# Kernel optimization log

Measured on AMD Instinct MI355X. Metric: run time of the kernel, lower is better.

The kernel has to match this reference:

```python
import jax, jax.numpy as jnp
import numpy as np

B, L, C, S, W, R = 2, 16, 64, 64, 128, 32
MOD_HIDDEN = 32


def _conv3d(x, k, b, pad_hw):
    # x: (B,C,L,S,W), k: (O,I,1,kh,kw)
    y = jax.lax.conv_general_dilated(
        x, k, window_strides=(1, 1, 1),
        padding=((0, 0), (pad_hw, pad_hw), (pad_hw, pad_hw)),
        dimension_numbers=('NCDHW', 'OIDHW', 'NCDHW'))
    return y + b[None, :, None, None, None]


def setup_inputs() -> dict:
    key = jax.random.key(0)
    ks = jax.random.split(key, 16)
    d = {}
    d['x'] = jax.random.normal(ks[0], (B, L, C, S, W), jnp.float32)
    u1 = jax.random.uniform(ks[1], (C, R), jnp.float32)
    u2 = jax.random.uniform(ks[2], (C, R), jnp.float32)
    r_min, r_max = 0.8, 0.99
    d['nu_log'] = jnp.log(-0.5 * jnp.log(u1 * (r_max ** 2 - r_min ** 2) + r_min ** 2))
    d['theta_log'] = jnp.log(u2 * jnp.float32(2 * np.pi))
    d['disp_nu'] = jnp.zeros((C, R), jnp.float32)
    d['disp_theta'] = jnp.zeros((C, R), jnp.float32)
    d['mlp_w1'] = jax.random.normal(ks[3], (C, MOD_HIDDEN), jnp.float32) / np.sqrt(C).astype(np.float32)
    d['mlp_b1'] = jnp.zeros((MOD_HIDDEN,), jnp.float32)
    d['mlp_w2'] = jax.random.normal(ks[4], (MOD_HIDDEN, C * R * 2), jnp.float32) / np.sqrt(MOD_HIDDEN).astype(np.float32)
    d['mlp_b2'] = jnp.zeros((C * R * 2,), jnp.float32)
    d['forcing_scale'] = jnp.float32(0.1)
    d['U_row_r'] = jax.random.normal(ks[5], (C, S, R), jnp.float32) / np.sqrt(S).astype(np.float32)
    d['U_row_i'] = jax.random.normal(ks[6], (C, S, R), jnp.float32) / np.sqrt(S).astype(np.float32)
    d['V_col_r'] = jax.random.normal(ks[7], (C, W, R), jnp.float32) / np.sqrt(W).astype(np.float32)
    d['V_col_i'] = jax.random.normal(ks[8], (C, W, R), jnp.float32) / np.sqrt(W).astype(np.float32)
    d['proj_W_r'] = jax.random.normal(ks[9], (C, C), jnp.float32) / np.sqrt(C).astype(np.float32)
    d['proj_W_i'] = jax.random.normal(ks[10], (C, C), jnp.float32) / np.sqrt(C).astype(np.float32)
    d['proj_b_r'] = jnp.zeros((C,), jnp.float32)
    d['proj_b_i'] = jnp.zeros((C,), jnp.float32)
    fan = np.sqrt(C * 9).astype(np.float32)
    d['convr_k'] = jax.random.normal(ks[11], (C, C, 1, 3, 3), jnp.float32) / fan
    d['convr_b'] = jnp.zeros((C,), jnp.float32)
    d['convi_k'] = jax.random.normal(ks[12], (C, C, 1, 3, 3), jnp.float32) / fan
    d['convi_b'] = jnp.zeros((C,), jnp.float32)
    d['fuse_k'] = jax.random.normal(ks[13], (C, 2 * C, 1, 1, 1), jnp.float32) / np.sqrt(2 * C).astype(np.float32)
    d['fuse_b'] = jnp.zeros((C,), jnp.float32)
    d['ln_g'] = jnp.ones((S, W), jnp.float32)
    d['ln_b'] = jnp.zeros((S, W), jnp.float32)
    return d


def reference(x, nu_log, theta_log, disp_nu, disp_theta, mlp_w1, mlp_b1,
              mlp_w2, mlp_b2, forcing_scale, U_row_r, U_row_i, V_col_r,
              V_col_i, proj_W_r, proj_W_i, proj_b_r, proj_b_i, convr_k,
              convr_b, convi_k, convi_b, fuse_k, fuse_b, ln_g, ln_b):
    # Diagonal LRU poles lam = exp(-exp(nu) + i*exp(theta)), per (C,R)
    nu = jnp.exp(nu_log + disp_nu)
    theta = jnp.exp(theta_log + disp_theta)
    lam = jnp.exp(jax.lax.complex(-nu, theta))
    gamma = jnp.sqrt(jnp.clip(1.0 - jnp.abs(lam) ** 2, 1e-6, None))

    # Selective input-dependent forcing from spatially-pooled context
    ctx = x.mean(axis=(-2, -1))  # (B,L,C)
    f = jnp.tanh(ctx @ mlp_w1 + mlp_b1) @ mlp_w2 + mlp_b2
    f = f.reshape(ctx.shape[0], ctx.shape[1], C, R, 2)
    forcing = forcing_scale * jax.lax.complex(f[..., 0], f[..., 1])  # (B,L,C,R)

    # Low-rank complex spatial projection to rank-R state per channel
    U = jax.lax.complex(U_row_r, U_row_i)  # (C,S,R)
    V = jax.lax.complex(V_col_r, V_col_i)  # (C,W,R)
    xc = x.astype(jnp.complex64)
    u = jnp.einsum('blcsw,csr->blcwr', xc, jnp.conj(U))
    u = jnp.einsum('blcwr,cwr->blcr', u, jnp.conj(V))  # (B,L,C,R)
    u = gamma * u * (1.0 + forcing)

    # Diagonal linear recurrence h_t = lam*h_{t-1} + u_t via associative scan over L
    A = jnp.broadcast_to(lam[None, None], u.shape)

    def comb(e1, e2):
        a1, b1 = e1
        a2, b2 = e2
        return a1 * a2, a2 * b1 + b2

    _, h = jax.lax.associative_scan(comb, (A, u), axis=1)

    # Reconstruct spatial field from low-rank states
    t = jnp.einsum('blcr,csr->blcsr', h, U)
    y = jnp.einsum('blcsr,cwr->blcsw', t, V)  # (B,L,C,S,W) complex

    projW = jax.lax.complex(proj_W_r, proj_W_i)
    projb = jax.lax.complex(proj_b_r, proj_b_i)
    y = jnp.einsum('blcsw,oc->blosw', y, projW) + projb[None, None, :, None, None]

    # Post-recurrence spatial convs on real/imag parts, fuse, layernorm, residual
    yr = jnp.transpose(jnp.real(y), (0, 2, 1, 3, 4))  # (B,C,L,S,W)
    yi = jnp.transpose(jnp.imag(y), (0, 2, 1, 3, 4))
    yr = _conv3d(yr, convr_k, convr_b, 1)
    yi = _conv3d(yi, convi_k, convi_b, 1)
    fused = _conv3d(jnp.concatenate([yr, yi], axis=1), fuse_k, fuse_b, 0)
    fused = jnp.transpose(fused, (0, 2, 1, 3, 4))  # (B,L,C,S,W)

    mu = fused.mean(axis=(-2, -1), keepdims=True)
    var = fused.var(axis=(-2, -1), keepdims=True)
    normed = (fused - mu) / jnp.sqrt(var + 1e-5) * ln_g + ln_b
    return normed + x
```

## Files before the change

### kernel.cpp

```cpp
#include <hip/hip_runtime.h>

typedef unsigned short u16;
typedef unsigned int u32;
typedef __attribute__((ext_vector_type(8))) short short8;
typedef __attribute__((ext_vector_type(4))) float f32x4;
typedef __attribute__((ext_vector_type(16))) float f32x16;

constexpr int B = 2, L = 16, C = 64, S = 64, W = 128, R = 32, MH = 32;
constexpr int BL = B * L;
constexpr int SW = S * W;
constexpr int CR = C * R;
constexpr int F2 = C * R * 2;
constexpr int NVE = 64 * 4 * 4 * 64 * 8;
constexpr int NVD = 64 * 8 * 2 * 64 * 8;

__device__ __forceinline__ float us2f(u16 h) { return __uint_as_float(((u32)h) << 16); }
__device__ __forceinline__ float bf_lo(u32 u) { return __uint_as_float(u << 16); }
__device__ __forceinline__ float bf_hi(u32 u) { return __uint_as_float(u & 0xffff0000u); }
__device__ __forceinline__ u16 f2bu(float f) {
  u32 u = __float_as_uint(f);
  u32 r = (u + 0x7fffu + ((u >> 16) & 1u)) >> 16;
  return (u16)r;
}
__device__ __forceinline__ u32 pack2(float lo, float hi) {
  return (u32)f2bu(lo) | ((u32)f2bu(hi) << 16);
}

__global__ void k_prep(const float* __restrict__ nu_log, const float* __restrict__ th_log,
                       const float* __restrict__ dnu, const float* __restrict__ dth,
                       float* __restrict__ lamr, float* __restrict__ lami,
                       float* __restrict__ gam) {
  int i = blockIdx.x * 256 + threadIdx.x;
  if (i >= CR) return;
  float nu = expf(nu_log[i] + dnu[i]);
  float th = expf(th_log[i] + dth[i]);
  float mag = expf(-nu);
  lamr[i] = mag * cosf(th);
  lami[i] = mag * sinf(th);
  gam[i] = sqrtf(fmaxf(1.0f - mag * mag, 1e-6f));
}

__global__ void k_keff(const float* __restrict__ fuse_k, const float* __restrict__ fuse_b,
                       const float* __restrict__ convr_k, const float* __restrict__ convr_b,
                       const float* __restrict__ convi_k, const float* __restrict__ convi_b,
                       u16* __restrict__ keff_bf, float* __restrict__ biaseff) {
  int i = blockIdx.x * 256 + threadIdx.x;
  if (i < C * 2 * C * 9) {
    int o = i / (2 * C * 9);
    int rem = i - o * (2 * C * 9);
    int cin2 = rem / 9;
    int seg = rem - cin2 * 9;
    const float* ck = (cin2 < C) ? convr_k : convi_k;
    int cin = cin2 & (C - 1);
    int fbase = o * 2 * C + ((cin2 < C) ? 0 : C);
    float acc = 0.f;
    for (int m = 0; m < C; ++m)
      acc += fuse_k[fbase + m] * ck[(m * C + cin) * 9 + seg];
    int kslice = cin2 >> 4;
    int kk = cin2 & 15;
    int lane = (o & 31) | ((kk >> 3) << 5);
    int j = kk & 7;
    int m_tile = o >> 5;
    keff_bf[((((seg * 8 + kslice) * 2 + m_tile) * 64 + lane) << 3) + j] = f2bu(acc);
  } else if (i < C * 2 * C * 9 + C) {
    int o = i - C * 2 * C * 9;
    float acc = fuse_b[o];
    for (int m = 0; m < C; ++m) {
      acc += fuse_k[o * 2 * C + m] * convr_b[m];
      acc += fuse_k[o * 2 * C + C + m] * convi_b[m];
    }
    biaseff[o] = acc;
  }
}

__global__ void k_vpack(const float* __restrict__ Vr, const float* __restrict__ Vi,
                        u16* __restrict__ venc, u16* __restrict__ vdecr,
                        u16* __restrict__ vdeci) {
  int i = blockIdx.x * 256 + threadIdx.x;
  if (i < NVE) {
    int j = i & 7, lane = (i >> 3) & 63, ks = (i >> 9) & 3;
    int wv = (i >> 11) & 3, c = i >> 13;
    int n = wv * 16 + (lane & 15);
    int w = ks * 32 + ((lane >> 4) & 3) * 8 + j;
    float v = (n < 32) ? Vr[(size_t)c * 4096 + w * 32 + n]
                       : -Vi[(size_t)c * 4096 + w * 32 + (n - 32)];
    venc[i] = f2bu(v);
  } else if (i < NVE + 2 * NVD) {
    int ii = i - NVE;
    int isI = 0;
    if (ii >= NVD) { ii -= NVD; isI = 1; }
    int j = ii & 7, lane = (ii >> 3) & 63, ks = (ii >> 9) & 1;
    int g = (ii >> 10) & 7, c = ii >> 13;
    int w = g * 16 + (lane & 15);
    int k = ks * 32 + ((lane >> 4) & 3) * 8 + j;
    float v;
    if (!isI) v = (k < 32) ? Vr[(size_t)c * 4096 + w * 32 + k]
                           : -Vi[(size_t)c * 4096 + w * 32 + (k - 32)];
    else      v = (k < 32) ? Vi[(size_t)c * 4096 + w * 32 + k]
                           :  Vr[(size_t)c * 4096 + w * 32 + (k - 32)];
    (isI ? vdeci : vdecr)[ii] = f2bu(v);
  }
}

__global__ void k_apack(const float* __restrict__ pWr, const float* __restrict__ pWi,
                        u16* __restrict__ aproj) {
  int i = blockIdx.x * 256 + threadIdx.x;
  if (i >= 128 * 128) return;
  int m = i >> 7, k = i & 127;
  int c = k >> 1, im = k & 1;
  int o = m & 63;
  float v;
  if (m < 64) v = im ? -pWi[o * 64 + c] : pWr[o * 64 + c];
  else        v = im ?  pWr[o * 64 + c] : pWi[o * 64 + c];
  aproj[i] = f2bu(v);
}

__global__ __launch_bounds__(256) void k_mlp(
    const float* __restrict__ ctx, const float* __restrict__ w1, const float* __restrict__ b1,
    const float* __restrict__ w2, const float* __restrict__ b2, const float* __restrict__ fscale,
    float* __restrict__ forcing) {
  int bl = blockIdx.x >> 4;
  int kt = blockIdx.x & 15;
  int k0 = kt * 256;
  __shared__ float cv[C];
  __shared__ float hid[MH];
  __shared__ float lw2[MH * 256];
  int t = threadIdx.x;
  if (t < C) cv[t] = ctx[bl * C + t];
  for (int i = t; i < MH * 64; i += 256) {
    int j = i >> 6, q = i & 63;
    ((float4*)lw2)[i] = ((const float4*)(w2 + (size_t)j * F2 + k0))[q];
  }
  __syncthreads();
  if (t < MH) {
    float a = b1[t];
    for (int c2 = 0; c2 < C; ++c2) a += cv[c2] * w1[c2 * MH + t];
    hid[t] = tanhf(a);
  }
  __syncthreads();
  float scale = fscale[0];
  float a = b2[k0 + t];
#pragma unroll
  for (int j = 0; j < MH; ++j) a += hid[j] * lw2[j * 256 + t];
  forcing[(size_t)bl * F2 + k0 + t] = scale * a;
}

__global__ __launch_bounds__(256) void k_enc(
    const float* __restrict__ x, const u16* __restrict__ venc,
    const float* __restrict__ Ur, const float* __restrict__ Ui,
    float* __restrict__ ctx, float* __restrict__ u) {
  int blc = blockIdx.x;
  int c = blc & (C - 1);
  __shared__ __align__(16) char smem[35968];
  u16* xt = (u16*)smem;
  float* uldr = (float*)(smem + 17408);
  float* uldi = uldr + 2048;
  float* y1  = (float*)smem;
  float* part = (float*)(smem + 33792);
  float* red = (float*)(smem + 35840);
  int t = threadIdx.x;
  int lane = t & 63, wv = t >> 6;
  short8 bf[4];
  {
    const short8* vep = (const short8*)venc + ((size_t)(c * 4 + wv) * 4) * 64 + lane;
#pragma unroll
    for (int ks = 0; ks < 4; ++ks) bf[ks] = vep[ks * 64];
  }
  float sm = 0.f;
  {
    const float4* xp = (const float4*)(x + (size_t)blc * SW);
    for (int i = t; i < SW / 4; i += 256) {
      float4 v = xp[i];
      sm += v.x + v.y + v.z + v.w;
      int idx = i * 4, s = idx >> 7, w = idx & 127;
      u32* d = (u32*)&xt[s * 136 + w];
      d[0] = pack2(v.x, v.y);
      d[1] = pack2(v.z, v.w);
    }
  }
#pragma unroll
  for (int o = 32; o > 0; o >>= 1) sm += __shfl_down(sm, o, 64);
  if (lane == 0) red[wv] = sm;
  {
    const float* urp = Ur + (size_t)c * 2048;
    const float* uip = Ui + (size_t)c * 2048;
    for (int i = t; i < 2048; i += 256) { uldr[i] = urp[i]; uldi[i] = uip[i]; }
  }
  __syncthreads();
  if (t == 0) ctx[blc] = (red[0] + red[1] + red[2] + red[3]) * (1.f / SW);
  int quad = lane >> 4, l15 = lane & 15;
  f32x4 zf = {0.f, 0.f, 0.f, 0.f};
  f32x4 acc[4] = {zf, zf, zf, zf};
#pragma unroll
  for (int ks = 0; ks < 4; ++ks) {
    int kofs = ks * 32 + quad * 8;
#pragma unroll
    for (int mt = 0; mt < 4; ++mt) {
      short8 af = *(const short8*)&xt[(mt * 16 + l15) * 136 + kofs];
      acc[mt] = __builtin_amdgcn_mfma_f32_16x16x32_bf16(af, bf[ks], acc[mt], 0, 0, 0);
    }
  }
  __syncthreads();
#pragma unroll
  for (int mt = 0; mt < 4; ++mt)
#pragma unroll
    for (int reg = 0; reg < 4; ++reg)
      y1[(mt * 16 + quad * 4 + reg) * 65 + wv * 16 + l15] = acc[mt][reg];
  __syncthreads();
  {
    int r = t & 31, sg = t >> 5;
    float pr = 0.f, pi = 0.f;
#pragma unroll
    for (int k = 0; k < 8; ++k) {
      int s = sg * 8 + k;
      float yr = y1[s * 65 + r], yi = y1[s * 65 + 32 + r];
      float ur = uldr[s * 32 + r], ui = uldi[s * 32 + r];
      pr += ur * yr + ui * yi;
      pi += ur * yi - ui * yr;
    }
    part[sg * 64 + r * 2]     = pr;
    part[sg * 64 + r * 2 + 1] = pi;
  }
  __syncthreads();
  if (t < 32) {
    float pr = 0.f, pi = 0.f;
#pragma unroll
    for (int sg = 0; sg < 8; ++sg) {
      pr += part[sg * 64 + t * 2];
      pi += part[sg * 64 + t * 2 + 1];
    }
    u[((size_t)blc * R + t) * 2]     = pr;
    u[((size_t)blc * R + t) * 2 + 1] = pi;
  }
}

__global__ void k_scan(const float* __restrict__ lamr, const float* __restrict__ lami,
                       const float* __restrict__ gam, const float* __restrict__ forcing,
                       const float* __restrict__ u, float* __restrict__ h) {
  int i = blockIdx.x * 256 + threadIdx.x;
  if (i >= B * CR) return;
  int b = i / CR;
  int cr = i - b * CR;
  float lr = lamr[cr], li = lami[cr], g = gam[cr];
  float hr = 0.f, hi = 0.f;
  for (int l = 0; l < L; ++l) {
    size_t off = ((size_t)(b * L + l) * CR + cr) * 2;
    float ur0 = u[off], ui0 = u[off + 1];
    float fr = forcing[off], fi = forcing[off + 1];
    float ofr = 1.f + fr;
    float ur = g * (ur0 * ofr - ui0 * fi);
    float ui = g * (ur0 * fi + ui0 * ofr);
    float nr = lr * hr - li * hi + ur;
    float ni = lr * hi + li * hr + ui;
    hr = nr; hi = ni;
    h[off] = hr; h[off + 1] = hi;
  }
}

__global__ __launch_bounds__(256) void k_decode(
    const float* __restrict__ h,
    const float* __restrict__ Ur, const float* __restrict__ Ui,
    const u16* __restrict__ vdecr, const u16* __restrict__ vdeci,
    u32* __restrict__ y_cm32, int bl_base) {
  int bid = blockIdx.x;
  int c = bid & 63;
  int blh = bid >> 6;
  int bl = bl_base + blh;
  __shared__ __align__(16) u16 ldA[64 * 72];
  int t = threadIdx.x;
  {
    const float* hp = h + ((size_t)(bl * C + c) * R) * 2;
    const float* urp = Ur + (size_t)c * (S * R);
    const float* uip = Ui + (size_t)c * (S * R);
    for (int p = t; p < S * R; p += 256) {
      int s = p >> 5, r = p & 31;
      float hr = hp[r * 2], hi = hp[r * 2 + 1];
      float ur = urp[p], ui = uip[p];
      ldA[s * 72 + r]      = f2bu(hr * ur - hi * ui);
      ldA[s * 72 + 32 + r] = f2bu(hr * ui + hi * ur);
    }
  }
  __syncthreads();
  int lane = t & 63, q = t >> 6;
  int quad = lane >> 4, l15 = lane & 15;
  const short8* vdr = (const short8*)vdecr + (size_t)c * 16 * 64;
  const short8* vdi = (const short8*)vdeci + (size_t)c * 16 * 64;
  f32x4 zf = {0.f, 0.f, 0.f, 0.f};
  f32x4 accr[4][2], acci[4][2];
#pragma unroll
  for (int mt = 0; mt < 4; ++mt)
#pragma unroll
    for (int nt = 0; nt < 2; ++nt) { accr[mt][nt] = zf; acci[mt][nt] = zf; }
#pragma unroll
  for (int ks = 0; ks < 2; ++ks) {
    int kofs = ks * 32 + quad * 8;
    short8 af[4];
#pragma unroll
    for (int mt = 0; mt < 4; ++mt)
      af[mt] = *(const short8*)&ldA[(mt * 16 + l15) * 72 + kofs];
#pragma unroll
    for (int nt = 0; nt < 2; ++nt) {
      int g = q * 2 + nt;
      short8 br = vdr[(g * 2 + ks) * 64 + lane];
      short8 bi = vdi[(g * 2 + ks) * 64 + lane];
#pragma unroll
      for (int mt = 0; mt < 4; ++mt) {
        accr[mt][nt] = __builtin_amdgcn_mfma_f32_16x16x32_bf16(af[mt], br, accr[mt][nt], 0, 0, 0);
        acci[mt][nt] = __builtin_amdgcn_mfma_f32_16x16x32_bf16(af[mt], bi, acci[mt][nt], 0, 0, 0);
      }
    }
  }
  u32* dst = y_cm32 + ((size_t)(blh * 64 + c) << 13);
#pragma unroll
  for (int mt = 0; mt < 4; ++mt) {
#pragma unroll
    for (int nt = 0; nt < 2; ++nt) {
      int w = q * 32 + nt * 16 + l15;
#pragma unroll
      for (int reg = 0; reg < 4; ++reg) {
        int s = mt * 16 + quad * 4 + reg;
        dst[s * 128 + w] = pack2(accr[mt][nt][reg], acci[mt][nt][reg]);
      }
    }
  }
}

__global__ __launch_bounds__(256) void k_proj(
    const u32* __restrict__ y_cm32, const u16* __restrict__ aproj,
    const float* __restrict__ pbr, const float* __restrict__ pbi,
    u16* __restrict__ ynhwc, int bl_base) {
  int bid = blockIdx.x;
  int ntile = bid & 15;
  int blh = bid >> 4;
  int bl = bl_base + blh;
  __shared__ __align__(16) u16 lda[128 * 136];
  __shared__ __align__(16) u32 ldb[128 * 68];
  __shared__ float ldbias[128];
  int t = threadIdx.x;
  for (int i = t; i < 128 * 16; i += 256) {
    int m = i >> 4, qq = i & 15;
    ((uint4*)&lda[m * 136])[qq] = ((const uint4*)&aproj[m * 128])[qq];
  }
  if (t < 128) ldbias[t] = t < 64 ? pbr[t] : pbi[t - 64];

  int lane = t & 63, wv = t >> 6;
  int quad = lane >> 4, l15 = lane & 15;
  int cidx = t & 63, seg = t >> 6;
  f32x4 zf = {0.f, 0.f, 0.f, 0.f};

  for (int chunk = 0; chunk < 4; ++chunk) {
    int n0 = ntile * 512 + chunk * 128;
    __syncthreads();
    {
      const uint4* src = (const uint4*)(y_cm32 + (((size_t)(blh * 64 + cidx)) << 13) + n0 + seg * 32);
      u32 tmp[32];
#pragma unroll
      for (int qq = 0; qq < 8; ++qq) {
        uint4 v = src[qq];
        tmp[qq * 4] = v.x; tmp[qq * 4 + 1] = v.y; tmp[qq * 4 + 2] = v.z; tmp[qq * 4 + 3] = v.w;
      }
#pragma unroll
      for (int j = 0; j < 32; ++j)
        ldb[(seg * 32 + j) * 68 + cidx] = tmp[j];
    }
    __syncthreads();
    f32x4 acc[8][2];
#pragma unroll
    for (int mt = 0; mt < 8; ++mt) { acc[mt][0] = zf; acc[mt][1] = zf; }
    const u16* ldb16 = (const u16*)ldb;
#pragma unroll
    for (int ks = 0; ks < 4; ++ks) {
      int kofs = ks * 32 + quad * 8;
      short8 af[8];
#pragma unroll
      for (int mt = 0; mt < 8; ++mt)
        af[mt] = *(const short8*)&lda[(mt * 16 + l15) * 136 + kofs];
#pragma unroll
      for (int nt = 0; nt < 2; ++nt) {
        int nrow = wv * 32 + nt * 16 + l15;
        short8 bf = *(const short8*)&ldb16[nrow * 136 + kofs];
#pragma unroll
        for (int mt = 0; mt < 8; ++mt)
          acc[mt][nt] = __builtin_amdgcn_mfma_f32_16x16x32_bf16(af[mt], bf, acc[mt][nt], 0, 0, 0);
      }
    }
#pragma unroll
    for (int nt = 0; nt < 2; ++nt) {
      int n = n0 + wv * 32 + nt * 16 + l15;
      u16* drow = ynhwc + (((size_t)bl * SW + n) << 7);
#pragma unroll
      for (int mt = 0; mt < 8; ++mt) {
        int ch = mt * 16 + quad * 4;
        u32 lo = pack2(acc[mt][nt][0] + ldbias[ch],     acc[mt][nt][1] + ldbias[ch + 1]);
        u32 hi = pack2(acc[mt][nt][2] + ldbias[ch + 2], acc[mt][nt][3] + ldbias[ch + 3]);
        u32* dp = (u32*)(drow + ch);
        dp[0] = lo; dp[1] = hi;
      }
    }
  }
}

__global__ __launch_bounds__(256, 4) void k_conv(
    const u16* __restrict__ ynhwc, const u16* __restrict__ keff_bf,
    const float* __restrict__ biaseff, u16* __restrict__ fused) {
  int bid = blockIdx.x;
  int wt = bid & 1;
  int st = (bid >> 1) & 31;
  int bl = bid >> 6;
  int s0 = st * 2;
  int w0 = wt * 64;
  __shared__ __align__(16) u16 win[4][66][72];
  int t = threadIdx.x;
  int c_lo = (wt == 0) ? 1 : 0;
  int c_hi = (wt == 0) ? 66 : 65;
  uint4 z4 = make_uint4(0u, 0u, 0u, 0u);

  int lane = t & 63;
  int wv = t >> 6;
  int sr = wv & 1;
  int mt = wv >> 1;
  int l31 = lane & 31, khalf = lane >> 5;

  f32x16 acc0, acc1;
#pragma unroll
  for (int i = 0; i < 16; ++i) { acc0[i] = 0.f; acc1[i] = 0.f; }
  const short8* ap = (const short8*)keff_bf;
  short8 abuf[2];

#pragma unroll
  for (int p = 0; p < 2; ++p) {
    if (p) __syncthreads();
    for (int rr = 0; rr < 4; ++rr) {
      int rs = s0 - 1 + rr;
      if (rs < 0 || rs >= S) {
        for (int i = t; i < 66 * 8; i += 256) {
          int col = i >> 3, q = i & 7;
          ((uint4*)&win[rr][col][0])[q] = z4;
        }
      } else {
        if (wt == 0 && t < 8) ((uint4*)&win[rr][0][0])[t] = z4;
        if (wt == 1 && t < 8) ((uint4*)&win[rr][65][0])[t] = z4;
        const uint4* src = (const uint4*)(ynhwc +
            (((size_t)bl * S + rs) * W + (w0 - 1 + c_lo)) * 128 + p * 64);
        int n4 = (c_hi - c_lo) * 8;
        for (int i = t; i < n4; i += 256) {
          int col = i >> 3, q = i & 7;
          ((uint4*)&win[rr][c_lo + col][0])[q] = src[col * 16 + q];
        }
      }
    }
    __syncthreads();

    abuf[0] = ap[((p * 4) * 2 + mt) * 64 + lane];

#pragma unroll
    for (int m = 0; m < 36; ++m) {
      const int cur = m & 1;
      const int nxt = cur ^ 1;
      if (m < 35) {
        const int m1 = m + 1;
        abuf[nxt] = ap[((((m1 >> 2) * 8 + p * 4 + (m1 & 3)) * 2 + mt)) * 64 + lane];
      }
      const int seg = m >> 2;
      const int k4 = m & 3;
      const int dr = seg / 3;
      const int dc = seg - dr * 3;
      const u16* bb = &win[sr + dr][l31 + dc][k4 * 16 + khalf * 8];
      short8 b0 = *(const short8*)bb;
      short8 b1 = *(const short8*)(bb + 32 * 72);
      acc0 = __builtin_amdgcn_mfma_f32_32x32x16_bf16(abuf[cur], b0, acc0, 0, 0, 0);
      acc1 = __builtin_amdgcn_mfma_f32_32x32x16_bf16(abuf[cur], b1, acc1, 0, 0, 0);
    }
  }

  int s_out = s0 + sr;
#pragma unroll
  for (int reg = 0; reg < 16; ++reg) {
    int o = mt * 32 + (reg & 3) + 8 * (reg >> 2) + 4 * khalf;
    float bias = biaseff[o];
    size_t rowoff = ((size_t)(bl * C + o) * S + s_out) * W;
    fused[rowoff + w0 + l31]      = f2bu(acc0[reg] + bias);
    fused[rowoff + w0 + 32 + l31] = f2bu(acc1[reg] + bias);
  }
}

__global__ __launch_bounds__(256) void k_ln(
    const u16* __restrict__ fused,
    const float* __restrict__ ln_g, const float* __restrict__ ln_b,
    const float* __restrict__ x, float* __restrict__ out) {
  int blc = blockIdx.x;
  __shared__ u16 fs[SW];
  __shared__ float red[12];
  int t = threadIdx.x;
  const uint4* fp = (const uint4*)(fused + (size_t)blc * SW);
  float sm = 0.f, sq = 0.f;
  for (int i = t; i < SW / 8; i += 256) {
    uint4 v = fp[i];
    ((uint4*)fs)[i] = v;
    float f0 = bf_lo(v.x), f1 = bf_hi(v.x), f2 = bf_lo(v.y), f3 = bf_hi(v.y);
    float f4 = bf_lo(v.z), f5 = bf_hi(v.z), f6 = bf_lo(v.w), f7 = bf_hi(v.w);
    sm += f0 + f1 + f2 + f3 + f4 + f5 + f6 + f7;
    sq += f0 * f0 + f1 * f1 + f2 * f2 + f3 * f3 + f4 * f4 + f5 * f5 + f6 * f6 + f7 * f7;
  }
#pragma unroll
  for (int off = 32; off > 0; off >>= 1) {
    sm += __shfl_down(sm, off, 64);
    sq += __shfl_down(sq, off, 64);
  }
  int lane = t & 63, wid = t >> 6;
  if (lane == 0) { red[wid * 2] = sm; red[wid * 2 + 1] = sq; }
  __syncthreads();
  if (t == 0) {
    float S1 = red[0] + red[2] + red[4] + red[6];
    float S2 = red[1] + red[3] + red[5] + red[7];
    float mu = S1 * (1.f / SW);
    float var = S2 * (1.f / SW) - mu * mu;
    red[8] = mu;
    red[9] = rsqrtf(var + 1e-5f);
  }
  __syncthreads();
  float mu = red[8], rstd = red[9];
  const float4* xp4 = (const float4*)(x + (size_t)blc * SW);
  float4* op4 = (float4*)(out + (size_t)blc * SW);
  const float4* g4 = (const float4*)ln_g;
  const float4* b4 = (const float4*)ln_b;
  const uint2* fs2 = (const uint2*)fs;
  for (int i = t; i < SW / 4; i += 256) {
    uint2 fv = fs2[i];
    float4 xv = xp4[i];
    float4 gv = g4[i];
    float4 bv = b4[i];
    float4 o;
    o.x = (bf_lo(fv.x) - mu) * rstd * gv.x + bv.x + xv.x;
    o.y = (bf_hi(fv.x) - mu) * rstd * gv.y + bv.y + xv.y;
    o.z = (bf_lo(fv.y) - mu) * rstd * gv.z + bv.z + xv.z;
    o.w = (bf_hi(fv.y) - mu) * rstd * gv.w + bv.w + xv.w;
    op4[i] = o;
  }
}

extern "C" void kernel_launch(void* const* d_in, const int* in_sizes, int n_in,
                              void* d_out, int out_size, void* d_ws, size_t ws_size,
                              hipStream_t stream) {
  (void)in_sizes; (void)n_in; (void)out_size; (void)ws_size;
  const float* x       = (const float*)d_in[0];
  const float* nu_log  = (const float*)d_in[1];
  const float* th_log  = (const float*)d_in[2];
  const float* dnu     = (const float*)d_in[3];
  const float* dth     = (const float*)d_in[4];
  const float* w1      = (const float*)d_in[5];
  const float* b1      = (const float*)d_in[6];
  const float* w2      = (const float*)d_in[7];
  const float* b2      = (const float*)d_in[8];
  const float* fscale  = (const float*)d_in[9];
  const float* Ur      = (const float*)d_in[10];
  const float* Ui      = (const float*)d_in[11];
  const float* Vr      = (const float*)d_in[12];
  const float* Vi      = (const float*)d_in[13];
  const float* pWr     = (const float*)d_in[14];
  const float* pWi     = (const float*)d_in[15];
  const float* pbr     = (const float*)d_in[16];
  const float* pbi     = (const float*)d_in[17];
  const float* convr_k = (const float*)d_in[18];
  const float* convr_b = (const float*)d_in[19];
  const float* convi_k = (const float*)d_in[20];
  const float* convi_b = (const float*)d_in[21];
  const float* fuse_k  = (const float*)d_in[22];
  const float* fuse_b  = (const float*)d_in[23];
  const float* ln_g    = (const float*)d_in[24];
  const float* ln_b    = (const float*)d_in[25];
  float* out = (float*)d_out;

  char* ws = (char*)d_ws;
  float* lamr    = (float*)ws;
  float* lami    = lamr + 2048;
  float* gam     = lami + 2048;
  float* biaseff = gam + 2048;
  float* ctx     = biaseff + 64;
  float* forcing = ctx + 2048;
  float* ubuf    = forcing + 131072;
  float* hbuf    = ubuf + 131072;
  u16* keff_bf   = (u16*)(hbuf + 131072);
  u16* aproj     = keff_bf + 73728;
  u16* venc      = aproj + 16384;
  u16* vdecr     = venc + NVE;
  u16* vdeci     = vdecr + NVD;
  size_t off = ((size_t)((char*)(vdeci + NVD) - ws) + 255) & ~(size_t)255;
  u32* y_cm32    = (u32*)(ws + off);
  u16* fused     = (u16*)y_cm32;
  u16* ynhwc     = (u16*)(ws + off + (size_t)32 * 1024 * 1024);

  k_prep<<<8, 256, 0, stream>>>(nu_log, th_log, dnu, dth, lamr, lami, gam);
  k_keff<<<289, 256, 0, stream>>>(fuse_k, fuse_b, convr_k, convr_b, convi_k, convi_b,
                                  keff_bf, biaseff);
  k_vpack<<<6144, 256, 0, stream>>>(Vr, Vi, venc, vdecr, vdeci);
  k_apack<<<64, 256, 0, stream>>>(pWr, pWi, aproj);
  k_enc<<<BL * C, 256, 0, stream>>>(x, venc, Ur, Ui, ctx, ubuf);
  k_mlp<<<BL * 16, 256, 0, stream>>>(ctx, w1, b1, w2, b2, fscale, forcing);
  k_scan<<<16, 256, 0, stream>>>(lamr, lami, gam, forcing, ubuf, hbuf);
  k_decode<<<1024, 256, 0, stream>>>(hbuf, Ur, Ui, vdecr, vdeci, y_cm32, 0);
  k_proj<<<256, 256, 0, stream>>>(y_cm32, aproj, pbr, pbi, ynhwc, 0);
  k_decode<<<1024, 256, 0, stream>>>(hbuf, Ur, Ui, vdecr, vdeci, y_cm32, 16);
  k_proj<<<256, 256, 0, stream>>>(y_cm32, aproj, pbr, pbi, ynhwc, 16);
  k_conv<<<2048, 256, 0, stream>>>(ynhwc, keff_bf, biaseff, fused);
  k_ln<<<BL * C, 256, 0, stream>>>(fused, ln_g, ln_b, x, out);
}
```

Before: 338.8 us.

## Merge prep kernels into one launch, stage scan through LDS, vectorize U loads

The four weight-preparation kernels are merged into a single launch that dispatches on block index, cutting three kernel launches. The scan kernel now stages u and forcing for a block of 128 channels into shared memory with coalesced loads, runs the recurrence from LDS, and writes h back coalesced, using 32 blocks instead of 16. The encoder's U loads switch to float4. Together these target launch overhead and uncoalesced strided access in the scan, at the cost of half the scan threads sitting idle during the recurrence.

```diff
diff --git a/kernel.cpp b/kernel.cpp
--- a/kernel.cpp
+++ b/kernel.cpp
@@ -14,6 +14,12 @@
 constexpr int NVE = 64 * 4 * 4 * 64 * 8;
 constexpr int NVD = 64 * 8 * 2 * 64 * 8;
 
+constexpr int NB_PREP  = 8;
+constexpr int NB_KEFF  = 289;
+constexpr int NB_APACK = 64;
+constexpr int NB_VPACK = (NVE + 2 * NVD + 255) / 256;
+constexpr int NB_ALL   = NB_PREP + NB_KEFF + NB_APACK + NB_VPACK;
+
 __device__ __forceinline__ float us2f(u16 h) { return __uint_as_float(((u32)h) << 16); }
 __device__ __forceinline__ float bf_lo(u32 u) { return __uint_as_float(u << 16); }
 __device__ __forceinline__ float bf_hi(u32 u) { return __uint_as_float(u & 0xffff0000u); }
@@ -26,93 +32,93 @@
   return (u32)f2bu(lo) | ((u32)f2bu(hi) << 16);
 }
 
-__global__ void k_prep(const float* __restrict__ nu_log, const float* __restrict__ th_log,
-                       const float* __restrict__ dnu, const float* __restrict__ dth,
-                       float* __restrict__ lamr, float* __restrict__ lami,
-                       float* __restrict__ gam) {
-  int i = blockIdx.x * 256 + threadIdx.x;
-  if (i >= CR) return;
-  float nu = expf(nu_log[i] + dnu[i]);
-  float th = expf(th_log[i] + dth[i]);
-  float mag = expf(-nu);
-  lamr[i] = mag * cosf(th);
-  lami[i] = mag * sinf(th);
-  gam[i] = sqrtf(fmaxf(1.0f - mag * mag, 1e-6f));
-}
-
-__global__ void k_keff(const float* __restrict__ fuse_k, const float* __restrict__ fuse_b,
-                       const float* __restrict__ convr_k, const float* __restrict__ convr_b,
-                       const float* __restrict__ convi_k, const float* __restrict__ convi_b,
-                       u16* __restrict__ keff_bf, float* __restrict__ biaseff) {
-  int i = blockIdx.x * 256 + threadIdx.x;
-  if (i < C * 2 * C * 9) {
-    int o = i / (2 * C * 9);
-    int rem = i - o * (2 * C * 9);
-    int cin2 = rem / 9;
-    int seg = rem - cin2 * 9;
-    const float* ck = (cin2 < C) ? convr_k : convi_k;
-    int cin = cin2 & (C - 1);
-    int fbase = o * 2 * C + ((cin2 < C) ? 0 : C);
-    float acc = 0.f;
-    for (int m = 0; m < C; ++m)
-      acc += fuse_k[fbase + m] * ck[(m * C + cin) * 9 + seg];
-    int kslice = cin2 >> 4;
-    int kk = cin2 & 15;
-    int lane = (o & 31) | ((kk >> 3) << 5);
-    int j = kk & 7;
-    int m_tile = o >> 5;
-    keff_bf[((((seg * 8 + kslice) * 2 + m_tile) * 64 + lane) << 3) + j] = f2bu(acc);
-  } else if (i < C * 2 * C * 9 + C) {
-    int o = i - C * 2 * C * 9;
-    float acc = fuse_b[o];
-    for (int m = 0; m < C; ++m) {
-      acc += fuse_k[o * 2 * C + m] * convr_b[m];
-      acc += fuse_k[o * 2 * C + C + m] * convi_b[m];
-    }
-    biaseff[o] = acc;
-  }
-}
-
-__global__ void k_vpack(const float* __restrict__ Vr, const float* __restrict__ Vi,
-                        u16* __restrict__ venc, u16* __restrict__ vdecr,
-                        u16* __restrict__ vdeci) {
-  int i = blockIdx.x * 256 + threadIdx.x;
-  if (i < NVE) {
-    int j = i & 7, lane = (i >> 3) & 63, ks = (i >> 9) & 3;
-    int wv = (i >> 11) & 3, c = i >> 13;
-    int n = wv * 16 + (lane & 15);
-    int w = ks * 32 + ((lane >> 4) & 3) * 8 + j;
-    float v = (n < 32) ? Vr[(size_t)c * 4096 + w * 32 + n]
-                       : -Vi[(size_t)c * 4096 + w * 32 + (n - 32)];
-    venc[i] = f2bu(v);
-  } else if (i < NVE + 2 * NVD) {
-    int ii = i - NVE;
-    int isI = 0;
-    if (ii >= NVD) { ii -= NVD; isI = 1; }
-    int j = ii & 7, lane = (ii >> 3) & 63, ks = (ii >> 9) & 1;
-    int g = (ii >> 10) & 7, c = ii >> 13;
-    int w = g * 16 + (lane & 15);
-    int k = ks * 32 + ((lane >> 4) & 3) * 8 + j;
+__global__ void k_prep_all(
+    const float* __restrict__ nu_log, const float* __restrict__ th_log,
+    const float* __restrict__ dnu, const float* __restrict__ dth,
+    float* __restrict__ lamr, float* __restrict__ lami, float* __restrict__ gam,
+    const float* __restrict__ fuse_k, const float* __restrict__ fuse_b,
+    const float* __restrict__ convr_k, const float* __restrict__ convr_b,
+    const float* __restrict__ convi_k, const float* __restrict__ convi_b,
+    u16* __restrict__ keff_bf, float* __restrict__ biaseff,
+    const float* __restrict__ pWr, const float* __restrict__ pWi,
+    u16* __restrict__ aproj,
+    const float* __restrict__ Vr, const float* __restrict__ Vi,
+    u16* __restrict__ venc, u16* __restrict__ vdecr, u16* __restrict__ vdeci) {
+  int bid = blockIdx.x;
+  int t = threadIdx.x;
+  if (bid < NB_PREP) {
+    int i = bid * 256 + t;
+    if (i >= CR) return;
+    float nu = expf(nu_log[i] + dnu[i]);
+    float th = expf(th_log[i] + dth[i]);
+    float mag = expf(-nu);
+    lamr[i] = mag * cosf(th);
+    lami[i] = mag * sinf(th);
+    gam[i] = sqrtf(fmaxf(1.0f - mag * mag, 1e-6f));
+  } else if (bid < NB_PREP + NB_KEFF) {
+    int i = (bid - NB_PREP) * 256 + t;
+    if (i < C * 2 * C * 9) {
+      int o = i / (2 * C * 9);
+      int rem = i - o * (2 * C * 9);
+      int cin2 = rem / 9;
+      int seg = rem - cin2 * 9;
+      const float* ck = (cin2 < C) ? convr_k : convi_k;
+      int cin = cin2 & (C - 1);
+      int fbase = o * 2 * C + ((cin2 < C) ? 0 : C);
+      float acc = 0.f;
+      for (int m = 0; m < C; ++m)
+        acc += fuse_k[fbase + m] * ck[(m * C + cin) * 9 + seg];
+      int kslice = cin2 >> 4;
+      int kk = cin2 & 15;
+      int lane = (o & 31) | ((kk >> 3) << 5);
+      int j = kk & 7;
+      int m_tile = o >> 5;
+      keff_bf[((((seg * 8 + kslice) * 2 + m_tile) * 64 + lane) << 3) + j] = f2bu(acc);
+    } else if (i < C * 2 * C * 9 + C) {
+      int o = i - C * 2 * C * 9;
+      float acc = fuse_b[o];
+      for (int m = 0; m < C; ++m) {
+        acc += fuse_k[o * 2 * C + m] * convr_b[m];
+        acc += fuse_k[o * 2 * C + C + m] * convi_b[m];
+      }
+      biaseff[o] = acc;
+    }
+  } else if (bid < NB_PREP + NB_KEFF + NB_APACK) {
+    int i = (bid - NB_PREP - NB_KEFF) * 256 + t;
+    if (i >= 128 * 128) return;
+    int m = i >> 7, k = i & 127;
+    int c = k >> 1, im = k & 1;
+    int o = m & 63;
     float v;
-    if (!isI) v = (k < 32) ? Vr[(size_t)c * 4096 + w * 32 + k]
-                           : -Vi[(size_t)c * 4096 + w * 32 + (k - 32)];
-    else      v = (k < 32) ? Vi[(size_t)c * 4096 + w * 32 + k]
-                           :  Vr[(size_t)c * 4096 + w * 32 + (k - 32)];
-    (isI ? vdeci : vdecr)[ii] = f2bu(v);
-  }
-}
-
-__global__ void k_apack(const float* __restrict__ pWr, const float* __restrict__ pWi,
-                        u16* __restrict__ aproj) {
-  int i = blockIdx.x * 256 + threadIdx.x;
-  if (i >= 128 * 128) return;
-  int m = i >> 7, k = i & 127;
-  int c = k >> 1, im = k & 1;
-  int o = m & 63;
-  float v;
-  if (m < 64) v = im ? -pWi[o * 64 + c] : pWr[o * 64 + c];
-  else        v = im ?  pWr[o * 64 + c] : pWi[o * 64 + c];
-  aproj[i] = f2bu(v);
+    if (m < 64) v = im ? -pWi[o * 64 + c] : pWr[o * 64 + c];
+    else        v = im ?  pWr[o * 64 + c] : pWi[o * 64 + c];
+    aproj[i] = f2bu(v);
+  } else {
+    int i = (bid - NB_PREP - NB_KEFF - NB_APACK) * 256 + t;
+    if (i < NVE) {
+      int j = i & 7, lane = (i >> 3) & 63, ks = (i >> 9) & 3;
+      int wv = (i >> 11) & 3, c = i >> 13;
+      int n = wv * 16 + (lane & 15);
+      int w = ks * 32 + ((lane >> 4) & 3) * 8 + j;
+      float v = (n < 32) ? Vr[(size_t)c * 4096 + w * 32 + n]
+                         : -Vi[(size_t)c * 4096 + w * 32 + (n - 32)];
+      venc[i] = f2bu(v);
+    } else if (i < NVE + 2 * NVD) {
+      int ii = i - NVE;
+      int isI = 0;
+      if (ii >= NVD) { ii -= NVD; isI = 1; }
+      int j = ii & 7, lane = (ii >> 3) & 63, ks = (ii >> 9) & 1;
+      int g = (ii >> 10) & 7, c = ii >> 13;
+      int w = g * 16 + (lane & 15);
+      int k = ks * 32 + ((lane >> 4) & 3) * 8 + j;
+      float v;
+      if (!isI) v = (k < 32) ? Vr[(size_t)c * 4096 + w * 32 + k]
+                             : -Vi[(size_t)c * 4096 + w * 32 + (k - 32)];
+      else      v = (k < 32) ? Vi[(size_t)c * 4096 + w * 32 + k]
+                             :  Vr[(size_t)c * 4096 + w * 32 + (k - 32)];
+      (isI ? vdeci : vdecr)[ii] = f2bu(v);
+    }
+  }
 }
 
 __global__ __launch_bounds__(256) void k_mlp(
@@ -182,9 +188,11 @@
   for (int o = 32; o > 0; o >>= 1) sm += __shfl_down(sm, o, 64);
   if (lane == 0) red[wv] = sm;
   {
-    const float* urp = Ur + (size_t)c * 2048;
-    const float* uip = Ui + (size_t)c * 2048;
-    for (int i = t; i < 2048; i += 256) { uldr[i] = urp[i]; uldi[i] = uip[i]; }
+    const float4* urp = (const float4*)(Ur + (size_t)c * 2048);
+    const float4* uip = (const float4*)(Ui + (size_t)c * 2048);
+    float4* dr = (float4*)uldr;
+    float4* di = (float4*)uldi;
+    for (int i = t; i < 512; i += 256) { dr[i] = urp[i]; di[i] = uip[i]; }
   }
   __syncthreads();
   if (t == 0) ctx[blc] = (red[0] + red[1] + red[2] + red[3]) * (1.f / SW);
@@ -234,26 +242,44 @@
   }
 }
 
-__global__ void k_scan(const float* __restrict__ lamr, const float* __restrict__ lami,
-                       const float* __restrict__ gam, const float* __restrict__ forcing,
-                       const float* __restrict__ u, float* __restrict__ h) {
-  int i = blockIdx.x * 256 + threadIdx.x;
-  if (i >= B * CR) return;
-  int b = i / CR;
-  int cr = i - b * CR;
-  float lr = lamr[cr], li = lami[cr], g = gam[cr];
-  float hr = 0.f, hi = 0.f;
+__global__ __launch_bounds__(256) void k_scan(
+    const float* __restrict__ lamr, const float* __restrict__ lami,
+    const float* __restrict__ gam, const float* __restrict__ forcing,
+    const float* __restrict__ u, float* __restrict__ h) {
+  int b = blockIdx.x >> 4;
+  int c0 = (blockIdx.x & 15) * 128;
+  __shared__ float uld[L][256];
+  __shared__ float fld[L][256];
+  int t = threadIdx.x;
+#pragma unroll
   for (int l = 0; l < L; ++l) {
-    size_t off = ((size_t)(b * L + l) * CR + cr) * 2;
-    float ur0 = u[off], ui0 = u[off + 1];
-    float fr = forcing[off], fi = forcing[off + 1];
-    float ofr = 1.f + fr;
-    float ur = g * (ur0 * ofr - ui0 * fi);
-    float ui = g * (ur0 * fi + ui0 * ofr);
-    float nr = lr * hr - li * hi + ur;
-    float ni = lr * hi + li * hr + ui;
-    hr = nr; hi = ni;
-    h[off] = hr; h[off + 1] = hi;
+    size_t base = ((size_t)(b * L + l) * CR + c0) * 2;
+    uld[l][t] = u[base + t];
+    fld[l][t] = forcing[base + t];
+  }
+  __syncthreads();
+  if (t < 128) {
+    int cr = c0 + t;
+    float lr = lamr[cr], li = lami[cr], g = gam[cr];
+    float hr = 0.f, hi = 0.f;
+#pragma unroll
+    for (int l = 0; l < L; ++l) {
+      float ur0 = uld[l][t * 2], ui0 = uld[l][t * 2 + 1];
+      float fr = fld[l][t * 2], fi = fld[l][t * 2 + 1];
+      float ofr = 1.f + fr;
+      float ur = g * (ur0 * ofr - ui0 * fi);
+      float ui = g * (ur0 * fi + ui0 * ofr);
+      float nr = lr * hr - li * hi + ur;
+      float ni = lr * hi + li * hr + ui;
+      hr = nr; hi = ni;
+      uld[l][t * 2] = hr; uld[l][t * 2 + 1] = hi;
+    }
+  }
+  __syncthreads();
+#pragma unroll
+  for (int l = 0; l < L; ++l) {
+    size_t base = ((size_t)(b * L + l) * CR + c0) * 2;
+    h[base + t] = uld[l][t];
   }
 }
 
@@ -590,14 +616,13 @@
   u16* fused     = (u16*)y_cm32;
   u16* ynhwc     = (u16*)(ws + off + (size_t)32 * 1024 * 1024);
 
-  k_prep<<<8, 256, 0, stream>>>(nu_log, th_log, dnu, dth, lamr, lami, gam);
-  k_keff<<<289, 256, 0, stream>>>(fuse_k, fuse_b, convr_k, convr_b, convi_k, convi_b,
-                                  keff_bf, biaseff);
-  k_vpack<<<6144, 256, 0, stream>>>(Vr, Vi, venc, vdecr, vdeci);
-  k_apack<<<64, 256, 0, stream>>>(pWr, pWi, aproj);
+  k_prep_all<<<NB_ALL, 256, 0, stream>>>(
+      nu_log, th_log, dnu, dth, lamr, lami, gam,
+      fuse_k, fuse_b, convr_k, convr_b, convi_k, convi_b, keff_bf, biaseff,
+      pWr, pWi, aproj, Vr, Vi, venc, vdecr, vdeci);
   k_enc<<<BL * C, 256, 0, stream>>>(x, venc, Ur, Ui, ctx, ubuf);
   k_mlp<<<BL * 16, 256, 0, stream>>>(ctx, w1, b1, w2, b2, fscale, forcing);
-  k_scan<<<16, 256, 0, stream>>>(lamr, lami, gam, forcing, ubuf, hbuf);
+  k_scan<<<32, 256, 0, stream>>>(lamr, lami, gam, forcing, ubuf, hbuf);
   k_decode<<<1024, 256, 0, stream>>>(hbuf, Ur, Ui, vdecr, vdeci, y_cm32, 0);
   k_proj<<<256, 256, 0, stream>>>(y_cm32, aproj, pbr, pbi, ynhwc, 0);
   k_decode<<<1024, 256, 0, stream>>>(hbuf, Ur, Ui, vdecr, vdeci, y_cm32, 16);
```

Result: no change. 332.5 us (-1.9%).
